# Kernel optimization log

Measured on AMD Instinct MI355X. Metric: run time of the kernel, lower is better.

## Reference

```python
import jax, jax.numpy as jnp
import numpy as np

H = 36   # num_heads
D = 32   # head_dim
C = 1152 # hidden_size (== H*D)


def setup_inputs() -> dict:
    key = jax.random.key(0)
    k1, k2, k3, k4 = jax.random.split(key, 4)
    B, N = 4, 8192
    x = jax.random.normal(k1, (B, N, C), dtype=jnp.float32)
    # torch Linear(hidden, 3*inner, bias=False): we store as (in, out) for x @ W
    W_qkv = jax.random.normal(k2, (C, 3 * H * D), dtype=jnp.float32) * (1.0 / np.sqrt(C))
    W_out = jax.random.normal(k3, (H * D, C), dtype=jnp.float32) * (1.0 / np.sqrt(H * D))
    b_out = jax.random.normal(k4, (C,), dtype=jnp.float32) * 0.01
    return {"x": x, "W_qkv": W_qkv, "W_out": W_out, "b_out": b_out}


def reference(x, W_qkv, W_out, b_out):
    B, N, _ = x.shape
    qkv = (x @ W_qkv).reshape(B, N, 3, H, D)
    q = jax.nn.relu(qkv[:, :, 0])  # (B,N,H,D)
    k = jax.nn.relu(qkv[:, :, 1])
    v = qkv[:, :, 2]
    # kv state: per-head (D,D) outer-product sum over tokens
    kv = jnp.einsum('bnhd,bnhe->bhde', k, v)        # (B,H,D,D)
    out = jnp.einsum('bnhd,bhde->bnhe', q, kv)      # (B,N,H,D)
    k_sum = k.sum(axis=1)                            # (B,H,D)
    denom = jnp.einsum('bnhd,bhd->bnh', q, k_sum)[..., None] + 1e-6
    out = (out / denom).reshape(B, N, H * D)
    return out @ W_out + b_out
```

## Files before the change

### kernel.cpp

```cpp
#include <hip/hip_runtime.h>
#include <hip/hip_bf16.h>
#include <stdint.h>


#define HH 36
#define DD 32
#define CC 1152
#define NB 4
#define NN 8192
#define M_TOT (NB * NN)
#define N1 (3 * HH * DD)
#define HD (HH * DD)
#define HPB 6

typedef __attribute__((ext_vector_type(8))) short bf16x8;
typedef __attribute__((ext_vector_type(4))) float f32x4;

__device__ __forceinline__ uint16_t f2b(float f) {
  union { float f; uint32_t u; } v; v.f = f;
  uint32_t u = v.u;
  return (uint16_t)((u + 0x7fffu + ((u >> 16) & 1u)) >> 16);
}
__device__ __forceinline__ float uasf(uint32_t u) {
  union { uint32_t u; float f; } v; v.u = u; return v.f;
}
__device__ __forceinline__ void unpack8v(uint4 u, f32x4& lo, f32x4& hi) {
  lo[0] = uasf(u.x << 16); lo[1] = uasf(u.x & 0xffff0000u);
  lo[2] = uasf(u.y << 16); lo[3] = uasf(u.y & 0xffff0000u);
  hi[0] = uasf(u.z << 16); hi[1] = uasf(u.z & 0xffff0000u);
  hi[2] = uasf(u.w << 16); hi[3] = uasf(u.w & 0xffff0000u);
}

#define GLOAD16(g, l)                                                        \
  __builtin_amdgcn_global_load_lds(                                          \
      (const __attribute__((address_space(1))) void*)(g),                    \
      (__attribute__((address_space(3))) void*)(l), 16, 0, 0)

__global__ void zero_kernel(float* __restrict__ p, int n) {
  int i = blockIdx.x * blockDim.x + threadIdx.x;
  if (i < n) p[i] = 0.f;
}

__global__ void convert_kernel(const float* __restrict__ in, uint16_t* __restrict__ out, int n4) {
  int i = blockIdx.x * blockDim.x + threadIdx.x;
  if (i >= n4) return;
  float4 v = ((const float4*)in)[i];
  ushort4 o;
  o.x = f2b(v.x); o.y = f2b(v.y); o.z = f2b(v.z); o.w = f2b(v.w);
  ((ushort4*)out)[i] = o;
}

__global__ void transpose_convert_kernel(const float* __restrict__ in, uint16_t* __restrict__ out,
                                         int R, int Cc) {
  __shared__ uint16_t tile[32][33];
  int c0 = blockIdx.x * 32, r0 = blockIdx.y * 32;
  int tx = threadIdx.x & 31, ty = threadIdx.x >> 5;
#pragma unroll
  for (int i = 0; i < 4; i++) {
    int r = ty + i * 8;
    tile[r][tx] = f2b(in[(size_t)(r0 + r) * Cc + c0 + tx]);
  }
  __syncthreads();
#pragma unroll
  for (int i = 0; i < 4; i++) {
    int c = ty + i * 8;
    out[(size_t)(c0 + c) * R + r0 + tx] = tile[tx][c];
  }
}

template <int EPI, int NC>
__global__ __launch_bounds__(256)
void gemm_bf16_kernel(const uint16_t* __restrict__ A, const uint16_t* __restrict__ BT,
                      uint16_t* __restrict__ outb, float* __restrict__ outf,
                      const float* __restrict__ bias, int K) {
  constexpr int NT = NC / 128;
  __shared__ uint16_t As[128 * 32];
  __shared__ uint16_t Bs[128 * 32];
  const int flat = blockIdx.y * NT + blockIdx.x;
  const int xcd = flat & 7;
  const int s = flat >> 3;
  const int n0 = (s % NT) * 128;
  const int m0 = ((s / NT) * 8 + xcd) * 128;
  const int t = threadIdx.x;
  const int lane = t & 63, w = t >> 6;
  const int wr = w >> 1, wc = w & 1;
  const int l15 = lane & 15, q4 = lane >> 4;
  f32x4 acc[4][4] = {};

  const int srow = w * 16 + (lane >> 2);
  const int sseg = (lane & 3) * 8;
  const uint16_t* Ag0 = A + (size_t)(m0 + srow) * K + sseg;
  const uint16_t* Ag1 = Ag0 + (size_t)64 * K;
  const uint16_t* Bg0 = BT + (size_t)(n0 + srow) * K + sseg;
  const uint16_t* Bg1 = Bg0 + (size_t)64 * K;
  uint16_t* lA0 = &As[(w * 16) * 32];
  uint16_t* lA1 = &As[(64 + w * 16) * 32];
  uint16_t* lB0 = &Bs[(w * 16) * 32];
  uint16_t* lB1 = &Bs[(64 + w * 16) * 32];
  const int aoff = q4 * 8;

  for (int k0 = 0; k0 < K; k0 += 32) {
    __syncthreads();
    GLOAD16(Ag0 + k0, lA0);
    GLOAD16(Ag1 + k0, lA1);
    GLOAD16(Bg0 + k0, lB0);
    GLOAD16(Bg1 + k0, lB1);
    __syncthreads();
    bf16x8 af[4], bfr[4];
#pragma unroll
    for (int i = 0; i < 4; i++) af[i] = *(const bf16x8*)&As[(wr * 64 + i * 16 + l15) * 32 + aoff];
#pragma unroll
    for (int j = 0; j < 4; j++) bfr[j] = *(const bf16x8*)&Bs[(wc * 64 + j * 16 + l15) * 32 + aoff];
#pragma unroll
    for (int i = 0; i < 4; i++)
#pragma unroll
      for (int j = 0; j < 4; j++)
        acc[i][j] = __builtin_amdgcn_mfma_f32_16x16x32_bf16(af[i], bfr[j], acc[i][j], 0, 0, 0);
  }
#pragma unroll
  for (int i = 0; i < 4; i++) {
#pragma unroll
    for (int j = 0; j < 4; j++) {
      int col = n0 + wc * 64 + j * 16 + l15;
#pragma unroll
      for (int r = 0; r < 4; r++) {
        int row = m0 + wr * 64 + i * 16 + q4 * 4 + r;
        float v = acc[i][j][r];
        if (EPI == 0) {
          if (col < 2 * HD) v = fmaxf(v, 0.f);
          outb[(size_t)row * NC + col] = f2b(v);
        } else {
          outf[(size_t)row * NC + col] = v + bias[col];
        }
      }
    }
  }
}

__global__ __launch_bounds__(64)
void kv_kernel(const uint16_t* __restrict__ qkvb, float* __restrict__ kvT, float* __restrict__ ksum) {
  __shared__ float kb[32][40];
  __shared__ float vb[32][40];
  const int bh = blockIdx.x >> 3;
  const int sp = blockIdx.x & 7;
  const int b = bh / HH, h = bh % HH;
  const int t = threadIdx.x;
  const int d0 = (t >> 3) * 4, e0 = (t & 7) * 4;
  const int m0 = b * NN + sp * (NN / 8);
  const size_t koff = (size_t)HD + h * DD;
  const size_t voff = (size_t)2 * HD + h * DD;
  float acc[4][4] = {};
  float ks[4] = {};
  const int srow = t >> 1, sseg = (t & 1) * 16;
  for (int c = 0; c < NN / 8; c += 32) {
    const uint16_t* kp = qkvb + (size_t)(m0 + c + srow) * N1 + koff + sseg;
    const uint16_t* vp = qkvb + (size_t)(m0 + c + srow) * N1 + voff + sseg;
    uint4 kr0 = *(const uint4*)kp;
    uint4 kr1 = *(const uint4*)(kp + 8);
    uint4 vr0 = *(const uint4*)vp;
    uint4 vr1 = *(const uint4*)(vp + 8);
    f32x4 klo, khi, klo2, khi2, vlo, vhi, vlo2, vhi2;
    unpack8v(kr0, klo, khi); unpack8v(kr1, klo2, khi2);
    unpack8v(vr0, vlo, vhi); unpack8v(vr1, vlo2, vhi2);
    __syncthreads();
    *(f32x4*)&kb[srow][sseg + 0] = klo;  *(f32x4*)&kb[srow][sseg + 4] = khi;
    *(f32x4*)&kb[srow][sseg + 8] = klo2; *(f32x4*)&kb[srow][sseg + 12] = khi2;
    *(f32x4*)&vb[srow][sseg + 0] = vlo;  *(f32x4*)&vb[srow][sseg + 4] = vhi;
    *(f32x4*)&vb[srow][sseg + 8] = vlo2; *(f32x4*)&vb[srow][sseg + 12] = vhi2;
    __syncthreads();
#pragma unroll 8
    for (int n = 0; n < 32; n++) {
      f32x4 kd = *(const f32x4*)&kb[n][d0];
      f32x4 ve = *(const f32x4*)&vb[n][e0];
#pragma unroll
      for (int i = 0; i < 4; i++)
#pragma unroll
        for (int j = 0; j < 4; j++) acc[i][j] += kd[i] * ve[j];
      if ((t & 7) == 0) {
#pragma unroll
        for (int i = 0; i < 4; i++) ks[i] += kd[i];
      }
    }
  }
#pragma unroll
  for (int i = 0; i < 4; i++)
#pragma unroll
    for (int j = 0; j < 4; j++)
      atomicAdd(&kvT[(size_t)bh * 1024 + (e0 + j) * DD + d0 + i], acc[i][j]);
  if ((t & 7) == 0) {
#pragma unroll
    for (int i = 0; i < 4; i++) atomicAdd(&ksum[bh * DD + d0 + i], ks[i]);
  }
}

__global__ __launch_bounds__(256)
void attn_kernel(const uint16_t* __restrict__ qkvb, const float* __restrict__ kvT,
                 const float* __restrict__ ksum, uint16_t* __restrict__ attn) {
  const int t = threadIdx.x;
  const int lane = t & 63, w = t >> 6;
  const int mbase = blockIdx.x * 256 + w * 64;
  const int b = mbase >> 13;
  const int e = lane & 31, dh = lane >> 5;
  const int h0 = blockIdx.y * HPB;
  for (int hh = 0; hh < HPB; hh++) {
    const int h = h0 + hh;
    const int bh = b * HH + h;
    const float* kvp = kvT + (size_t)bh * 1024 + e * DD + dh * 16;
    f32x4 kva = *(const f32x4*)(kvp + 0);
    f32x4 kvb2 = *(const f32x4*)(kvp + 4);
    f32x4 kvc = *(const f32x4*)(kvp + 8);
    f32x4 kvd = *(const f32x4*)(kvp + 12);
    const float* ksp = ksum + bh * DD + dh * 16;
    f32x4 ksa = *(const f32x4*)(ksp + 0);
    f32x4 ksb = *(const f32x4*)(ksp + 4);
    f32x4 ksc = *(const f32x4*)(ksp + 8);
    f32x4 ksd = *(const f32x4*)(ksp + 12);
#pragma unroll 4
    for (int r = 0; r < 64; r++) {
      const int m = mbase + r;
      const uint16_t* qp = qkvb + (size_t)m * N1 + h * DD + dh * 16;
      uint4 q0 = *(const uint4*)qp;
      uint4 q1 = *(const uint4*)(qp + 8);
      f32x4 qa, qb2, qc, qd;
      unpack8v(q0, qa, qb2);
      unpack8v(q1, qc, qd);
      float o = 0.f, den = 0.f;
#pragma unroll
      for (int ii = 0; ii < 4; ii++) {
        o += qa[ii] * kva[ii];  den += qa[ii] * ksa[ii];
        o += qb2[ii] * kvb2[ii]; den += qb2[ii] * ksb[ii];
        o += qc[ii] * kvc[ii];  den += qc[ii] * ksc[ii];
        o += qd[ii] * kvd[ii];  den += qd[ii] * ksd[ii];
      }
      o += __shfl_xor(o, 32);
      den += __shfl_xor(den, 32);
      float res = o / (den + 1e-6f);
      if (dh == 0) attn[(size_t)m * HD + h * DD + e] = f2b(res);
    }
  }
}

extern "C" void kernel_launch(void* const* d_in, const int* in_sizes, int n_in,
                              void* d_out, int out_size, void* d_ws, size_t ws_size,
                              hipStream_t stream) {
  const float* x = (const float*)d_in[0];
  const float* Wqkv = (const float*)d_in[1];
  const float* Wout = (const float*)d_in[2];
  const float* bout = (const float*)d_in[3];
  float* y = (float*)d_out;
  char* ws = (char*)d_ws;
  uint16_t* xb = (uint16_t*)ws;
  uint16_t* wqkvT = (uint16_t*)(ws + 75497472);
  uint16_t* woutT = (uint16_t*)(ws + 83460096);
  uint16_t* qkvb = (uint16_t*)(ws + 86114304);
  float* kvT = (float*)(ws + 312606720);
  float* ksum = (float*)(ws + 313196544);
  uint16_t* attn = xb;

  zero_kernel<<<(152064 + 255) / 256, 256, 0, stream>>>(kvT, 152064);
  convert_kernel<<<(M_TOT * CC / 4) / 256, 256, 0, stream>>>(x, xb, M_TOT * CC / 4);
  transpose_convert_kernel<<<dim3(N1 / 32, CC / 32), 256, 0, stream>>>(Wqkv, wqkvT, CC, N1);
  transpose_convert_kernel<<<dim3(CC / 32, CC / 32), 256, 0, stream>>>(Wout, woutT, CC, CC);
  gemm_bf16_kernel<0, N1><<<dim3(N1 / 128, M_TOT / 128), 256, 0, stream>>>(xb, wqkvT, qkvb, nullptr, nullptr, CC);
  kv_kernel<<<144 * 8, 64, 0, stream>>>(qkvb, kvT, ksum);
  attn_kernel<<<dim3(M_TOT / 256, HH / HPB), 256, 0, stream>>>(qkvb, kvT, ksum, attn);
  gemm_bf16_kernel<1, CC><<<dim3(CC / 128, M_TOT / 128), 256, 0, stream>>>(attn, woutT, nullptr, y, bout, CC);
}
```

Before: 1.033 ms.

## Deepen GEMM K-tile with XOR-swizzled LDS, widen KV split, shrink attn heads

The GEMM now stages a 64-wide K slice per iteration, halving the number of barrier pairs per tile. It uses an XOR swizzle on the 16-byte segments to avoid LDS bank conflicts on the MFMA fragment reads, and gets a launch-bounds occupancy hint. Separately, the KV reduction is split across 32 sequence chunks instead of 8 to expose more blocks, and the attention kernel handles 3 heads per block instead of 6 for more parallelism. The trade-offs are double the LDS per GEMM block, more atomic partial sums in the KV stage, and less reuse per attention block.

```diff
diff --git a/kernel.cpp b/kernel.cpp
--- a/kernel.cpp
+++ b/kernel.cpp
@@ -11,7 +11,8 @@
 #define M_TOT (NB * NN)
 #define N1 (3 * HH * DD)
 #define HD (HH * DD)
-#define HPB 6
+#define HPB 3
+#define KVSPLIT 32
 
 typedef __attribute__((ext_vector_type(8))) short bf16x8;
 typedef __attribute__((ext_vector_type(4))) float f32x4;
@@ -69,13 +70,13 @@
 }
 
 template <int EPI, int NC>
-__global__ __launch_bounds__(256)
+__global__ __launch_bounds__(256, 4)
 void gemm_bf16_kernel(const uint16_t* __restrict__ A, const uint16_t* __restrict__ BT,
                       uint16_t* __restrict__ outb, float* __restrict__ outf,
                       const float* __restrict__ bias, int K) {
   constexpr int NT = NC / 128;
-  __shared__ uint16_t As[128 * 32];
-  __shared__ uint16_t Bs[128 * 32];
+  __shared__ uint16_t As[128 * 64];
+  __shared__ uint16_t Bs[128 * 64];
   const int flat = blockIdx.y * NT + blockIdx.x;
   const int xcd = flat & 7;
   const int s = flat >> 3;
@@ -87,35 +88,41 @@
   const int l15 = lane & 15, q4 = lane >> 4;
   f32x4 acc[4][4] = {};
 
-  const int srow = w * 16 + (lane >> 2);
-  const int sseg = (lane & 3) * 8;
-  const uint16_t* Ag0 = A + (size_t)(m0 + srow) * K + sseg;
-  const uint16_t* Ag1 = Ag0 + (size_t)64 * K;
-  const uint16_t* Bg0 = BT + (size_t)(n0 + srow) * K + sseg;
-  const uint16_t* Bg1 = Bg0 + (size_t)64 * K;
-  uint16_t* lA0 = &As[(w * 16) * 32];
-  uint16_t* lA1 = &As[(64 + w * 16) * 32];
-  uint16_t* lB0 = &Bs[(w * 16) * 32];
-  uint16_t* lB1 = &Bs[(64 + w * 16) * 32];
-  const int aoff = q4 * 8;
-
-  for (int k0 = 0; k0 < K; k0 += 32) {
-    __syncthreads();
-    GLOAD16(Ag0 + k0, lA0);
-    GLOAD16(Ag1 + k0, lA1);
-    GLOAD16(Bg0 + k0, lB0);
-    GLOAD16(Bg1 + k0, lB1);
-    __syncthreads();
-    bf16x8 af[4], bfr[4];
-#pragma unroll
-    for (int i = 0; i < 4; i++) af[i] = *(const bf16x8*)&As[(wr * 64 + i * 16 + l15) * 32 + aoff];
-#pragma unroll
-    for (int j = 0; j < 4; j++) bfr[j] = *(const bf16x8*)&Bs[(wc * 64 + j * 16 + l15) * 32 + aoff];
-#pragma unroll
-    for (int i = 0; i < 4; i++)
-#pragma unroll
-      for (int j = 0; j < 4; j++)
-        acc[i][j] = __builtin_amdgcn_mfma_f32_16x16x32_bf16(af[i], bfr[j], acc[i][j], 0, 0, 0);
+  const int srow = w * 32 + (lane >> 3);
+  const int sseg = ((lane & 7) ^ (lane >> 3)) * 8;
+  const uint16_t* Ag = A + (size_t)(m0 + srow) * K + sseg;
+  const uint16_t* Bg = BT + (size_t)(n0 + srow) * K + sseg;
+  uint16_t* lA = &As[(w * 32) * 64];
+  uint16_t* lB = &Bs[(w * 32) * 64];
+
+  for (int k0 = 0; k0 < K; k0 += 64) {
+    __syncthreads();
+#pragma unroll
+    for (int i = 0; i < 4; i++) {
+      GLOAD16(Ag + k0 + (size_t)(i * 8) * K, lA + i * 8 * 64);
+      GLOAD16(Bg + k0 + (size_t)(i * 8) * K, lB + i * 8 * 64);
+    }
+    __syncthreads();
+#pragma unroll
+    for (int kk = 0; kk < 2; kk++) {
+      bf16x8 af[4], bfr[4];
+      const int sbase = (kk * 4 + q4);
+#pragma unroll
+      for (int i = 0; i < 4; i++) {
+        const int row = wr * 64 + i * 16 + l15;
+        af[i] = *(const bf16x8*)&As[row * 64 + (sbase ^ (l15 & 7)) * 8];
+      }
+#pragma unroll
+      for (int j = 0; j < 4; j++) {
+        const int row = wc * 64 + j * 16 + l15;
+        bfr[j] = *(const bf16x8*)&Bs[row * 64 + (sbase ^ (l15 & 7)) * 8];
+      }
+#pragma unroll
+      for (int i = 0; i < 4; i++)
+#pragma unroll
+        for (int j = 0; j < 4; j++)
+          acc[i][j] = __builtin_amdgcn_mfma_f32_16x16x32_bf16(af[i], bfr[j], acc[i][j], 0, 0, 0);
+    }
   }
 #pragma unroll
   for (int i = 0; i < 4; i++) {
@@ -141,18 +148,18 @@
 void kv_kernel(const uint16_t* __restrict__ qkvb, float* __restrict__ kvT, float* __restrict__ ksum) {
   __shared__ float kb[32][40];
   __shared__ float vb[32][40];
-  const int bh = blockIdx.x >> 3;
-  const int sp = blockIdx.x & 7;
+  const int bh = blockIdx.x / KVSPLIT;
+  const int sp = blockIdx.x % KVSPLIT;
   const int b = bh / HH, h = bh % HH;
   const int t = threadIdx.x;
   const int d0 = (t >> 3) * 4, e0 = (t & 7) * 4;
-  const int m0 = b * NN + sp * (NN / 8);
+  const int m0 = b * NN + sp * (NN / KVSPLIT);
   const size_t koff = (size_t)HD + h * DD;
   const size_t voff = (size_t)2 * HD + h * DD;
   float acc[4][4] = {};
   float ks[4] = {};
   const int srow = t >> 1, sseg = (t & 1) * 16;
-  for (int c = 0; c < NN / 8; c += 32) {
+  for (int c = 0; c < NN / KVSPLIT; c += 32) {
     const uint16_t* kp = qkvb + (size_t)(m0 + c + srow) * N1 + koff + sseg;
     const uint16_t* vp = qkvb + (size_t)(m0 + c + srow) * N1 + voff + sseg;
     uint4 kr0 = *(const uint4*)kp;
@@ -262,7 +269,7 @@
   transpose_convert_kernel<<<dim3(N1 / 32, CC / 32), 256, 0, stream>>>(Wqkv, wqkvT, CC, N1);
   transpose_convert_kernel<<<dim3(CC / 32, CC / 32), 256, 0, stream>>>(Wout, woutT, CC, CC);
   gemm_bf16_kernel<0, N1><<<dim3(N1 / 128, M_TOT / 128), 256, 0, stream>>>(xb, wqkvT, qkvb, nullptr, nullptr, CC);
-  kv_kernel<<<144 * 8, 64, 0, stream>>>(qkvb, kvT, ksum);
+  kv_kernel<<<144 * KVSPLIT, 64, 0, stream>>>(qkvb, kvT, ksum);
   attn_kernel<<<dim3(M_TOT / 256, HH / HPB), 256, 0, stream>>>(qkvb, kvT, ksum, attn);
   gemm_bf16_kernel<1, CC><<<dim3(CC / 128, M_TOT / 128), 256, 0, stream>>>(attn, woutT, nullptr, y, bout, CC);
 }
```

Result: faster. 957.7 us (-7.3%).
